# Optimization experiments

Hardware: AMD Instinct MI355X
Metric: run time of the kernel (lower is better)

Reference implementation:

```python
import jax, jax.numpy as jnp
import numpy as np

B, N, D = 2, 2048, 1024
H = 16
DH = D // H

def setup_inputs() -> dict:
    key = jax.random.key(0)
    ks = jax.random.split(key, 9)
    s = 1.0 / np.sqrt(D)
    return {
        "x": jax.random.normal(ks[0], (B, N, D), dtype=jnp.float32),
        "Wq": jax.random.uniform(ks[1], (D, D), jnp.float32, -s, s),
        "bq": jax.random.uniform(ks[2], (D,), jnp.float32, -s, s),
        "Wk": jax.random.uniform(ks[3], (D, D), jnp.float32, -s, s),
        "bk": jax.random.uniform(ks[4], (D,), jnp.float32, -s, s),
        "Wv": jax.random.uniform(ks[5], (D, D), jnp.float32, -s, s),
        "bv": jax.random.uniform(ks[6], (D,), jnp.float32, -s, s),
        "Wo": jax.random.uniform(ks[7], (D, D), jnp.float32, -s, s),
        "bo": jax.random.uniform(ks[8], (D,), jnp.float32, -s, s),
    }

def reference(x, Wq, bq, Wk, bk, Wv, bv, Wo, bo):
    # torch Linear: y = x @ W.T + b
    scale = 1.0 / np.sqrt(DH)
    q = (x @ Wq.T + bq).reshape(B, N, H, DH).transpose(0, 2, 1, 3)  # [B,H,N,DH]
    k = (x @ Wk.T + bk).reshape(B, N, H, DH).transpose(0, 2, 1, 3)
    v = (x @ Wv.T + bv).reshape(B, N, H, DH).transpose(0, 2, 1, 3)
    scores = jnp.einsum('bhnd,bhmd->bhnm', q, k) * scale  # [B,H,N,N]
    attn = jax.nn.softmax(scores, axis=-1)
    out = jnp.einsum('bhnm,bhmd->bhnd', attn, v)  # [B,H,N,DH]
    out = out.transpose(0, 2, 1, 3).reshape(B, N, D)
    return out @ Wo.T + bo
```

## Files before the change

### kernel.cpp

```cpp
#include <hip/hip_runtime.h>
#include <hip/hip_bf16.h>

#define B_  2
#define N_  2048
#define D_  1024
#define H_  16
#define DH_ 64
#define BN_ (B_*N_)

typedef __attribute__((ext_vector_type(8))) short short8;
typedef __attribute__((ext_vector_type(4))) short short4v;
typedef __attribute__((ext_vector_type(4))) float f32x4;
typedef __attribute__((ext_vector_type(16))) float f32x16;

typedef __attribute__((address_space(3))) unsigned int lds_u32_t;
typedef const __attribute__((address_space(1))) unsigned int glb_u32_t;

__device__ __forceinline__ void async_load16(const unsigned short* g, unsigned short* l) {
    __builtin_amdgcn_global_load_lds((glb_u32_t*)g, (lds_u32_t*)l, 16, 0, 0);
}

__device__ __forceinline__ unsigned short f2bf(float f) {
    __hip_bfloat16 h = __float2bfloat16(f);
    return *reinterpret_cast<unsigned short*>(&h);
}

__device__ __forceinline__ unsigned int pkbf(float a, float b) {
    unsigned int ua = __float_as_uint(a) + 0x8000u;
    unsigned int ub = __float_as_uint(b) + 0x8000u;
    return __builtin_amdgcn_perm(ub, ua, 0x07060302);
}

#if __has_builtin(__builtin_amdgcn_exp2f)
#define EXP2(x) __builtin_amdgcn_exp2f(x)
#else
#define EXP2(x) exp2f(x)
#endif

#define QSCL 0.1803368801111204f

__global__ __launch_bounds__(256) void cast_kernel(
    const float* __restrict__ x,  const float* __restrict__ wq,
    const float* __restrict__ wk, const float* __restrict__ wv,
    const float* __restrict__ wo,
    unsigned short* __restrict__ xb,  unsigned short* __restrict__ wqb,
    unsigned short* __restrict__ wkb, unsigned short* __restrict__ wvb,
    unsigned short* __restrict__ wob)
{
    const size_t NX = (size_t)BN_ * D_;
    const size_t NW = (size_t)D_ * D_;
    size_t i = ((size_t)blockIdx.x * 256 + threadIdx.x) * 4;
    const float* src; unsigned short* dst; size_t off;
    if (i < NX) { src = x; dst = xb; off = i; }
    else {
        size_t j = (i - NX) >> 20;
        off = (i - NX) & (NW - 1);
        src = (j == 0) ? wq : (j == 1) ? wk : (j == 2) ? wv : wo;
        dst = (j == 0) ? wqb : (j == 1) ? wkb : (j == 2) ? wvb : wob;
    }
    float4 v = *(const float4*)(src + off);
    ushort4 o;
    o.x = f2bf(v.x); o.y = f2bf(v.y); o.z = f2bf(v.z); o.w = f2bf(v.w);
    *(ushort4*)(dst + off) = o;
}

template<int OUT_MODE>
__device__ __forceinline__ void gemm_body(
    unsigned short* __restrict__ As, unsigned short* __restrict__ Bs,
    const unsigned short* __restrict__ A, const unsigned short* __restrict__ W,
    const float* __restrict__ bias, void* __restrict__ Cout, int bx, int by)
{
    constexpr int K = D_;
    const int tid  = threadIdx.x;
    const int lane = tid & 63;
    const int wave = tid >> 6;
    const int wm = wave & 1, wn = wave >> 1;
    const int l15 = lane & 15, quad = lane >> 4;

    f32x4 acc[4][4] = {};
    const int row0 = by * 128, col0 = bx * 128;

    const int srow = lane >> 3;
    const int scb  = lane & 7;

    for (int k0 = 0; k0 < K; k0 += 64) {
        __syncthreads();
#pragma unroll
        for (int cc = 0; cc < 4; ++cc) {
            int c  = wave * 4 + cc;
            int lr = c * 8 + srow;
            int gcol = k0 + ((scb ^ (lr & 7)) * 8);
            async_load16(A + (size_t)(row0 + lr) * K + gcol, As + c * 512);
            async_load16(W + (size_t)(col0 + lr) * K + gcol, Bs + c * 512);
        }
        __syncthreads();

#pragma unroll
        for (int kf = 0; kf < 2; ++kf) {
            const int swz = ((kf * 4 + quad) ^ (l15 & 7)) * 8;
            short8 af[4], bf[4];
#pragma unroll
            for (int mi = 0; mi < 4; mi++)
                af[mi] = *(const short8*)(&As[(wm * 64 + mi * 16 + l15) * 64 + swz]);
#pragma unroll
            for (int ni = 0; ni < 4; ni++)
                bf[ni] = *(const short8*)(&Bs[(wn * 64 + ni * 16 + l15) * 64 + swz]);
#pragma unroll
            for (int mi = 0; mi < 4; mi++)
#pragma unroll
                for (int ni = 0; ni < 4; ni++)
                    acc[mi][ni] = __builtin_amdgcn_mfma_f32_16x16x32_bf16(
                        af[mi], bf[ni], acc[mi][ni], 0, 0, 0);
        }
    }

#pragma unroll
    for (int ni = 0; ni < 4; ni++) {
        int col = col0 + wn * 64 + ni * 16 + l15;
        float bv = bias[col];
#pragma unroll
        for (int mi = 0; mi < 4; mi++) {
            int row = row0 + wm * 64 + mi * 16 + quad * 4;
            if (OUT_MODE == 2) {
                ushort4 pk;
                pk.x = f2bf(acc[mi][ni][0] + bv);
                pk.y = f2bf(acc[mi][ni][1] + bv);
                pk.z = f2bf(acc[mi][ni][2] + bv);
                pk.w = f2bf(acc[mi][ni][3] + bv);
                *(ushort4*)((unsigned short*)Cout + (size_t)col * BN_ + row) = pk;
            } else {
#pragma unroll
                for (int r = 0; r < 4; r++) {
                    float v = acc[mi][ni][r] + bv;
                    if (OUT_MODE == 3) v *= QSCL;
                    if (OUT_MODE == 0)
                        ((float*)Cout)[(size_t)(row + r) * D_ + col] = v;
                    else
                        ((unsigned short*)Cout)[(size_t)(row + r) * D_ + col] = f2bf(v);
                }
            }
        }
    }
}

__global__ __launch_bounds__(256) void qkv_gemm(
    const unsigned short* __restrict__ xb,
    const unsigned short* __restrict__ wqb, const unsigned short* __restrict__ wkb,
    const unsigned short* __restrict__ wvb,
    const float* __restrict__ bq, const float* __restrict__ bk, const float* __restrict__ bv,
    unsigned short* __restrict__ q, unsigned short* __restrict__ k, unsigned short* __restrict__ vt)
{
    __shared__ __align__(16) unsigned short As[128 * 64];
    __shared__ __align__(16) unsigned short Bs[128 * 64];
    if (blockIdx.z == 0)
        gemm_body<3>(As, Bs, xb, wqb, bq, q,  blockIdx.x, blockIdx.y);
    else if (blockIdx.z == 1)
        gemm_body<1>(As, Bs, xb, wkb, bk, k,  blockIdx.x, blockIdx.y);
    else
        gemm_body<2>(As, Bs, xb, wvb, bv, vt, blockIdx.x, blockIdx.y);
}

__global__ __launch_bounds__(256) void out_gemm(
    const unsigned short* __restrict__ attn, const unsigned short* __restrict__ wob,
    const float* __restrict__ bo, float* __restrict__ out)
{
    __shared__ __align__(16) unsigned short As[128 * 64];
    __shared__ __align__(16) unsigned short Bs[128 * 64];
    gemm_body<0>(As, Bs, attn, wob, bo, out, blockIdx.x, blockIdx.y);
}

__global__ __launch_bounds__(256) void attn_kernel(
    const unsigned short* __restrict__ q, const unsigned short* __restrict__ k,
    const unsigned short* __restrict__ vt, unsigned short* __restrict__ o)
{
    __shared__ __align__(16) unsigned short Ks[64 * 64];
    __shared__ __align__(16) unsigned short Vs[64 * 64];
    __shared__ __align__(16) unsigned short Ps[4][32 * 72];

    const int tid = threadIdx.x;
    const int lane = tid & 63, wave = tid >> 6;
    const int l31 = lane & 31, kq = lane >> 5;
    const int bh = blockIdx.x;
    const int qt = blockIdx.y;
    const int b = bh >> 4, h = bh & 15;

    const unsigned short* qb = q  + (size_t)b * N_ * D_ + h * DH_;
    const unsigned short* kb = k  + (size_t)b * N_ * D_ + h * DH_;
    const unsigned short* vb = vt + (size_t)h * DH_ * BN_ + (size_t)b * N_;

    const int qrow0 = qt * 128 + wave * 32;

    short8 qf[4];
#pragma unroll
    for (int s = 0; s < 4; s++)
        qf[s] = *(const short8*)(qb + (size_t)(qrow0 + l31) * D_ + s * 16 + kq * 8);

    f32x16 oacc[2] = {};
    f32x16 lacc = {};

    short8 onesf;
#pragma unroll
    for (int j = 0; j < 8; j++) onesf[j] = (short)0x3F80;

    char* Pw = (char*)Ps[wave];
    const int pswz = (l31 >> 3) & 3;
    const int srow = lane >> 3, scb = lane & 7;

    for (int kv0 = 0; kv0 < N_; kv0 += 64) {
        __syncthreads();
#pragma unroll
        for (int cc = 0; cc < 2; ++cc) {
            int c  = wave * 2 + cc;
            int lr = c * 8 + srow;
            int swz8 = (scb ^ (lr & 7)) * 8;
            async_load16(kb + (size_t)(kv0 + lr) * D_ + swz8, (unsigned short*)Ks + c * 512);
            async_load16(vb + (size_t)lr * BN_ + kv0 + swz8,  (unsigned short*)Vs + c * 512);
        }
        __syncthreads();

        f32x16 st[2] = {};
#pragma unroll
        for (int s = 0; s < 4; s++) {
#pragma unroll
            for (int mb = 0; mb < 2; mb++) {
                short8 kfr = *(const short8*)((const char*)Ks +
                    (mb * 32 + l31) * 128 + (((2 * s + kq) ^ (l31 & 7)) * 16));
                st[mb] = __builtin_amdgcn_mfma_f32_32x32x16_bf16(
                    kfr, qf[s], st[mb], 0, 0, 0);
            }
        }

#pragma unroll
        for (int mb = 0; mb < 2; mb++) {
#pragma unroll
            for (int g = 0; g < 4; g++) {
                float p0 = EXP2(st[mb][g * 4 + 0]);
                float p1 = EXP2(st[mb][g * 4 + 1]);
                float p2 = EXP2(st[mb][g * 4 + 2]);
                float p3 = EXP2(st[mb][g * 4 + 3]);
                uint2 val;
                val.x = pkbf(p0, p1);
                val.y = pkbf(p2, p3);
                int ib = (mb * 8 + g * 2 + kq) ^ (pswz * 2);
                *(short4v*)(Pw + l31 * 144 + ib * 8) = __builtin_bit_cast(short4v, val);
            }
        }

        asm volatile("s_waitcnt lgkmcnt(0)" ::: "memory");

#pragma unroll
        for (int s = 0; s < 4; s++) {
            short8 pf = *(const short8*)(Pw + l31 * 144 + (((2 * s + kq) ^ pswz) * 16));
#pragma unroll
            for (int nb = 0; nb < 2; nb++) {
                short8 vf = *(const short8*)((const char*)Vs +
                    (nb * 32 + l31) * 128 + (((2 * s + kq) ^ (l31 & 7)) * 16));
                oacc[nb] = __builtin_amdgcn_mfma_f32_32x32x16_bf16(pf, vf, oacc[nb], 0, 0, 0);
            }
            lacc = __builtin_amdgcn_mfma_f32_32x32x16_bf16(pf, onesf, lacc, 0, 0, 0);
        }
    }

#pragma unroll
    for (int g = 0; g < 4; g++)
#pragma unroll
        for (int rr = 0; rr < 4; rr++) {
            int reg = g * 4 + rr;
            float inv = 1.f / lacc[reg];
            int row = qrow0 + rr + 8 * g + 4 * kq;
            size_t base = ((size_t)b * N_ + row) * D_ + h * DH_;
#pragma unroll
            for (int nb = 0; nb < 2; nb++)
                o[base + nb * 32 + l31] = f2bf(oacc[nb][reg] * inv);
        }
}

extern "C" void kernel_launch(void* const* d_in, const int* in_sizes, int n_in,
                              void* d_out, int out_size, void* d_ws, size_t ws_size,
                              hipStream_t stream)
{
    const float* x  = (const float*)d_in[0];
    const float* Wq = (const float*)d_in[1];
    const float* bq = (const float*)d_in[2];
    const float* Wk = (const float*)d_in[3];
    const float* bk = (const float*)d_in[4];
    const float* Wv = (const float*)d_in[5];
    const float* bv = (const float*)d_in[6];
    const float* Wo = (const float*)d_in[7];
    const float* bo = (const float*)d_in[8];
    float* out = (float*)d_out;

    char* ws = (char*)d_ws;
    unsigned short* xb  = (unsigned short*)(ws + 0);
    unsigned short* wqb = (unsigned short*)(ws + 8388608);
    unsigned short* wkb = (unsigned short*)(ws + 10485760);
    unsigned short* wvb = (unsigned short*)(ws + 12582912);
    unsigned short* wob = (unsigned short*)(ws + 14680064);
    unsigned short* qd  = (unsigned short*)(ws + 16777216);
    unsigned short* kd  = (unsigned short*)(ws + 25165824);
    unsigned short* vtd = (unsigned short*)(ws + 33554432);
    unsigned short* ad  = (unsigned short*)(ws + 41943040);

    cast_kernel<<<8192, 256, 0, stream>>>(x, Wq, Wk, Wv, Wo, xb, wqb, wkb, wvb, wob);
    qkv_gemm<<<dim3(8, 32, 3), 256, 0, stream>>>(xb, wqb, wkb, wvb, bq, bk, bv, qd, kd, vtd);
    attn_kernel<<<dim3(32, 16), 256, 0, stream>>>(qd, kd, vtd, ad);
    out_gemm<<<dim3(8, 32), 256, 0, stream>>>(ad, wob, bo, out);
}
```

Before: 210.4 us.

## Split KV range across wave pairs and feed P from registers into PV MFMA

The attention kernel now handles 64 query rows per block, with two wave pairs each processing half of the KV sequence into separate double LDS buffers. Partial O and row-sum accumulators are merged through LDS at the end. The P tile is no longer written to and reread from LDS. Its register layout feeds directly into 32x32x8 MFMAs, which removes the Ps buffer and its wait. The grid doubles to 1024 blocks for more parallelism, at the cost of smaller-K MFMAs, twice as many K/V loads per query, and a reduction epilogue.

```diff
diff --git a/kernel.cpp b/kernel.cpp
--- a/kernel.cpp
+++ b/kernel.cpp
@@ -173,13 +173,13 @@
     const unsigned short* __restrict__ q, const unsigned short* __restrict__ k,
     const unsigned short* __restrict__ vt, unsigned short* __restrict__ o)
 {
-    __shared__ __align__(16) unsigned short Ks[64 * 64];
-    __shared__ __align__(16) unsigned short Vs[64 * 64];
-    __shared__ __align__(16) unsigned short Ps[4][32 * 72];
+    __shared__ __align__(16) unsigned short Ks[2][64 * 64];
+    __shared__ __align__(16) unsigned short Vs[2][64 * 64];
 
     const int tid = threadIdx.x;
     const int lane = tid & 63, wave = tid >> 6;
     const int l31 = lane & 31, kq = lane >> 5;
+    const int pair = wave >> 1, wrow = wave & 1;
     const int bh = blockIdx.x;
     const int qt = blockIdx.y;
     const int b = bh >> 4, h = bh & 15;
@@ -188,7 +188,7 @@
     const unsigned short* kb = k  + (size_t)b * N_ * D_ + h * DH_;
     const unsigned short* vb = vt + (size_t)h * DH_ * BN_ + (size_t)b * N_;
 
-    const int qrow0 = qt * 128 + wave * 32;
+    const int qrow0 = qt * 64 + wrow * 32;
 
     short8 qf[4];
 #pragma unroll
@@ -198,32 +198,35 @@
     f32x16 oacc[2] = {};
     f32x16 lacc = {};
 
-    short8 onesf;
-#pragma unroll
-    for (int j = 0; j < 8; j++) onesf[j] = (short)0x3F80;
-
-    char* Pw = (char*)Ps[wave];
-    const int pswz = (l31 >> 3) & 3;
+    short4v ones4;
+#pragma unroll
+    for (int j = 0; j < 4; j++) ones4[j] = (short)0x3F80;
+
     const int srow = lane >> 3, scb = lane & 7;
-
-    for (int kv0 = 0; kv0 < N_; kv0 += 64) {
+    const int kvbase = pair * (N_ / 2);
+
+    for (int it = 0; it < N_ / 128; ++it) {
+        const int kv0 = kvbase + it * 64;
         __syncthreads();
 #pragma unroll
-        for (int cc = 0; cc < 2; ++cc) {
-            int c  = wave * 2 + cc;
+        for (int cc = 0; cc < 4; ++cc) {
+            int c  = wrow * 4 + cc;
             int lr = c * 8 + srow;
             int swz8 = (scb ^ (lr & 7)) * 8;
-            async_load16(kb + (size_t)(kv0 + lr) * D_ + swz8, (unsigned short*)Ks + c * 512);
-            async_load16(vb + (size_t)lr * BN_ + kv0 + swz8,  (unsigned short*)Vs + c * 512);
+            async_load16(kb + (size_t)(kv0 + lr) * D_ + swz8, (unsigned short*)Ks[pair] + c * 512);
+            async_load16(vb + (size_t)lr * BN_ + kv0 + swz8,  (unsigned short*)Vs[pair] + c * 512);
         }
         __syncthreads();
 
+        const unsigned short* Kc = Ks[pair];
+        const unsigned short* Vc = Vs[pair];
+
         f32x16 st[2] = {};
 #pragma unroll
         for (int s = 0; s < 4; s++) {
 #pragma unroll
             for (int mb = 0; mb < 2; mb++) {
-                short8 kfr = *(const short8*)((const char*)Ks +
+                short8 kfr = *(const short8*)((const char*)Kc +
                     (mb * 32 + l31) * 128 + (((2 * s + kq) ^ (l31 & 7)) * 16));
                 st[mb] = __builtin_amdgcn_mfma_f32_32x32x16_bf16(
                     kfr, qf[s], st[mb], 0, 0, 0);
@@ -241,38 +244,54 @@
                 uint2 val;
                 val.x = pkbf(p0, p1);
                 val.y = pkbf(p2, p3);
-                int ib = (mb * 8 + g * 2 + kq) ^ (pswz * 2);
-                *(short4v*)(Pw + l31 * 144 + ib * 8) = __builtin_bit_cast(short4v, val);
+                short4v pf = __builtin_bit_cast(short4v, val);
+#pragma unroll
+                for (int nb = 0; nb < 2; nb++) {
+                    short4v vf = *(const short4v*)((const char*)Vc +
+                        (nb * 32 + l31) * 128 + (((mb * 4 + g) ^ (l31 & 7)) * 16) + kq * 8);
+                    oacc[nb] = __builtin_amdgcn_mfma_f32_32x32x8bf16_1k(
+                        pf, vf, oacc[nb], 0, 0, 0);
+                }
+                lacc = __builtin_amdgcn_mfma_f32_32x32x8bf16_1k(
+                    pf, ones4, lacc, 0, 0, 0);
             }
         }
-
-        asm volatile("s_waitcnt lgkmcnt(0)" ::: "memory");
-
-#pragma unroll
-        for (int s = 0; s < 4; s++) {
-            short8 pf = *(const short8*)(Pw + l31 * 144 + (((2 * s + kq) ^ pswz) * 16));
-#pragma unroll
-            for (int nb = 0; nb < 2; nb++) {
-                short8 vf = *(const short8*)((const char*)Vs +
-                    (nb * 32 + l31) * 128 + (((2 * s + kq) ^ (l31 & 7)) * 16));
-                oacc[nb] = __builtin_amdgcn_mfma_f32_32x32x16_bf16(pf, vf, oacc[nb], 0, 0, 0);
+    }
+
+    float* MO = (float*)&Ks[0][0];
+    float* ML = (float*)&Vs[0][0];
+    const int idx = wrow * 64 + lane;
+
+    __syncthreads();
+    if (pair == 1) {
+#pragma unroll
+        for (int s = 0; s < 16; s++) {
+            MO[s * 128 + idx]        = oacc[0][s];
+            MO[(16 + s) * 128 + idx] = oacc[1][s];
+            ML[s * 128 + idx]        = lacc[s];
+        }
+    }
+    __syncthreads();
+    if (pair == 0) {
+#pragma unroll
+        for (int s = 0; s < 16; s++) {
+            oacc[0][s] += MO[s * 128 + idx];
+            oacc[1][s] += MO[(16 + s) * 128 + idx];
+            lacc[s]    += ML[s * 128 + idx];
+        }
+#pragma unroll
+        for (int g = 0; g < 4; g++)
+#pragma unroll
+            for (int rr = 0; rr < 4; rr++) {
+                int reg = g * 4 + rr;
+                float inv = 1.f / lacc[reg];
+                int row = qrow0 + rr + 8 * g + 4 * kq;
+                size_t base = ((size_t)b * N_ + row) * D_ + h * DH_;
+#pragma unroll
+                for (int nb = 0; nb < 2; nb++)
+                    o[base + nb * 32 + l31] = f2bf(oacc[nb][reg] * inv);
             }
-            lacc = __builtin_amdgcn_mfma_f32_32x32x16_bf16(pf, onesf, lacc, 0, 0, 0);
-        }
-    }
-
-#pragma unroll
-    for (int g = 0; g < 4; g++)
-#pragma unroll
-        for (int rr = 0; rr < 4; rr++) {
-            int reg = g * 4 + rr;
-            float inv = 1.f / lacc[reg];
-            int row = qrow0 + rr + 8 * g + 4 * kq;
-            size_t base = ((size_t)b * N_ + row) * D_ + h * DH_;
-#pragma unroll
-            for (int nb = 0; nb < 2; nb++)
-                o[base + nb * 32 + l31] = f2bf(oacc[nb][reg] * inv);
-        }
+    }
 }
 
 extern "C" void kernel_launch(void* const* d_in, const int* in_sizes, int n_in,
@@ -303,6 +322,6 @@
 
     cast_kernel<<<8192, 256, 0, stream>>>(x, Wq, Wk, Wv, Wo, xb, wqb, wkb, wvb, wob);
     qkv_gemm<<<dim3(8, 32, 3), 256, 0, stream>>>(xb, wqb, wkb, wvb, bq, bk, bv, qd, kd, vtd);
-    attn_kernel<<<dim3(32, 16), 256, 0, stream>>>(qd, kd, vtd, ad);
+    attn_kernel<<<dim3(32, 32), 256, 0, stream>>>(qd, kd, vtd, ad);
     out_gemm<<<dim3(8, 32), 256, 0, stream>>>(ad, wob, bo, out);
 }
```

Result: slower. 216.8 us (+3.0%).

## Double-buffer K/V tiles and feed P directly from registers into MFMA

Applied to the files above, without the earlier changes.

Adds a second K/V LDS buffer so the next tile's async loads overlap the current tile's compute, which removes one barrier per iteration. The softmax probabilities now go straight from the S accumulator registers into 32x32x8 MFMAs, with no LDS round-trip. The row sum becomes a scalar register accumulation plus a cross-lane shuffle instead of an extra MFMA against ones. This relies on the S output layout matching the A-operand layout of the smaller MFMA and uses twice as many half-depth MFMA instructions for P·V.

```diff
diff --git a/kernel.cpp b/kernel.cpp
--- a/kernel.cpp
+++ b/kernel.cpp
@@ -173,9 +173,8 @@
     const unsigned short* __restrict__ q, const unsigned short* __restrict__ k,
     const unsigned short* __restrict__ vt, unsigned short* __restrict__ o)
 {
-    __shared__ __align__(16) unsigned short Ks[64 * 64];
-    __shared__ __align__(16) unsigned short Vs[64 * 64];
-    __shared__ __align__(16) unsigned short Ps[4][32 * 72];
+    __shared__ __align__(16) unsigned short Ks[2][64 * 64];
+    __shared__ __align__(16) unsigned short Vs[2][64 * 64];
 
     const int tid = threadIdx.x;
     const int lane = tid & 63, wave = tid >> 6;
@@ -196,34 +195,38 @@
         qf[s] = *(const short8*)(qb + (size_t)(qrow0 + l31) * D_ + s * 16 + kq * 8);
 
     f32x16 oacc[2] = {};
-    f32x16 lacc = {};
-
-    short8 onesf;
-#pragma unroll
-    for (int j = 0; j < 8; j++) onesf[j] = (short)0x3F80;
-
-    char* Pw = (char*)Ps[wave];
-    const int pswz = (l31 >> 3) & 3;
+    float lsum = 0.f;
+
     const int srow = lane >> 3, scb = lane & 7;
 
-    for (int kv0 = 0; kv0 < N_; kv0 += 64) {
-        __syncthreads();
+    auto stage = [&](int bi, int kv0) {
 #pragma unroll
         for (int cc = 0; cc < 2; ++cc) {
             int c  = wave * 2 + cc;
             int lr = c * 8 + srow;
             int swz8 = (scb ^ (lr & 7)) * 8;
-            async_load16(kb + (size_t)(kv0 + lr) * D_ + swz8, (unsigned short*)Ks + c * 512);
-            async_load16(vb + (size_t)lr * BN_ + kv0 + swz8,  (unsigned short*)Vs + c * 512);
-        }
+            async_load16(kb + (size_t)(kv0 + lr) * D_ + swz8, (unsigned short*)Ks[bi] + c * 512);
+            async_load16(vb + (size_t)lr * BN_ + kv0 + swz8,  (unsigned short*)Vs[bi] + c * 512);
+        }
+    };
+
+    stage(0, 0);
+
+    const int NIT = N_ / 64;
+    for (int it = 0; it < NIT; ++it) {
+        const int cur = it & 1;
         __syncthreads();
+        if (it + 1 < NIT) stage(cur ^ 1, (it + 1) * 64);
+
+        const unsigned short* Kc = Ks[cur];
+        const unsigned short* Vc = Vs[cur];
 
         f32x16 st[2] = {};
 #pragma unroll
         for (int s = 0; s < 4; s++) {
 #pragma unroll
             for (int mb = 0; mb < 2; mb++) {
-                short8 kfr = *(const short8*)((const char*)Ks +
+                short8 kfr = *(const short8*)((const char*)Kc +
                     (mb * 32 + l31) * 128 + (((2 * s + kq) ^ (l31 & 7)) * 16));
                 st[mb] = __builtin_amdgcn_mfma_f32_32x32x16_bf16(
                     kfr, qf[s], st[mb], 0, 0, 0);
@@ -238,35 +241,34 @@
                 float p1 = EXP2(st[mb][g * 4 + 1]);
                 float p2 = EXP2(st[mb][g * 4 + 2]);
                 float p3 = EXP2(st[mb][g * 4 + 3]);
+                lsum += (p0 + p1) + (p2 + p3);
                 uint2 val;
                 val.x = pkbf(p0, p1);
                 val.y = pkbf(p2, p3);
-                int ib = (mb * 8 + g * 2 + kq) ^ (pswz * 2);
-                *(short4v*)(Pw + l31 * 144 + ib * 8) = __builtin_bit_cast(short4v, val);
+                short4v pf = __builtin_bit_cast(short4v, val);
+#pragma unroll
+                for (int nb = 0; nb < 2; nb++) {
+                    short4v vf = *(const short4v*)((const char*)Vc +
+                        (nb * 32 + l31) * 128 + (((mb * 4 + g) ^ (l31 & 7)) * 16) + kq * 8);
+                    oacc[nb] = __builtin_amdgcn_mfma_f32_32x32x8bf16_1k(
+                        pf, vf, oacc[nb], 0, 0, 0);
+                }
             }
         }
-
-        asm volatile("s_waitcnt lgkmcnt(0)" ::: "memory");
-
-#pragma unroll
-        for (int s = 0; s < 4; s++) {
-            short8 pf = *(const short8*)(Pw + l31 * 144 + (((2 * s + kq) ^ pswz) * 16));
-#pragma unroll
-            for (int nb = 0; nb < 2; nb++) {
-                short8 vf = *(const short8*)((const char*)Vs +
-                    (nb * 32 + l31) * 128 + (((2 * s + kq) ^ (l31 & 7)) * 16));
-                oacc[nb] = __builtin_amdgcn_mfma_f32_32x32x16_bf16(pf, vf, oacc[nb], 0, 0, 0);
-            }
-            lacc = __builtin_amdgcn_mfma_f32_32x32x16_bf16(pf, onesf, lacc, 0, 0, 0);
-        }
     }
+
+    lsum += __shfl_xor(lsum, 32);
+    __syncthreads();
+    float* Lt = (float*)&Ks[0][0] + wave * 32;
+    if (kq == 0) Lt[l31] = lsum;
+    asm volatile("s_waitcnt lgkmcnt(0)" ::: "memory");
 
 #pragma unroll
     for (int g = 0; g < 4; g++)
 #pragma unroll
         for (int rr = 0; rr < 4; rr++) {
             int reg = g * 4 + rr;
-            float inv = 1.f / lacc[reg];
+            float inv = 1.f / Lt[rr + 8 * g + 4 * kq];
             int row = qrow0 + rr + 8 * g + 4 * kq;
             size_t base = ((size_t)b * N_ + row) * D_ + h * DH_;
 #pragma unroll
```

Result: no change. 210.4 us (-0.0%).
